# Performance work log

Measured on AMD Instinct MI355X. Metric: run time of the kernel, lower is better.

Reference implementation:

```python
import jax, jax.numpy as jnp
import numpy as np

B, T, C, H = 8, 2048, 1024, 128  # batch, seq (== block_size), embed_size, head_size


def setup_inputs() -> dict:
    key = jax.random.key(0)
    k1, k2, k3, k4 = jax.random.split(key, 4)
    x = jax.random.normal(k1, (B, T, C), dtype=jnp.float32)
    s = 1.0 / np.sqrt(C).astype(np.float32)
    Wq = jax.random.normal(k2, (C, H), dtype=jnp.float32) * s
    Wk = jax.random.normal(k3, (C, H), dtype=jnp.float32) * s
    Wv = jax.random.normal(k4, (C, H), dtype=jnp.float32) * s
    return {"x": x, "Wq": Wq, "Wk": Wk, "Wv": Wv}


def reference(x, Wq, Wk, Wv):
    # x: (B, T, C); projections are bias-free Linears -> x @ W
    Bs, Ts, Cs = x.shape
    q = x @ Wq  # (B, T, H)
    k = x @ Wk  # (B, T, H)
    v = x @ Wv  # (B, T, H)
    # NOTE: original scales by embed_size C ** -0.5, not head_size.
    sims = jnp.einsum('bth,bsh->bts', q, k) * (float(Cs) ** -0.5)  # (B, T, T)
    causal = jnp.tril(jnp.ones((Ts, Ts), dtype=bool))
    sims = jnp.where(causal[None, :, :], sims, -jnp.inf)
    attentions = jax.nn.softmax(sims, axis=-1)  # (B, T, T)
    return attentions @ v  # (B, T, H)
```

## Files before the change

kernel.cpp:

```cpp
#include <hip/hip_runtime.h>


#define B_ 8
#define T_ 2048
#define C_ 1024
#define H_ 128

typedef __attribute__((ext_vector_type(4))) float  f32x4;
typedef __attribute__((ext_vector_type(8))) __bf16 bf16x8;
typedef __attribute__((ext_vector_type(4))) __bf16 bf16x4;
typedef __attribute__((ext_vector_type(4))) short  short4v;

#define QSCALE (0.03125f * 1.44269504088896340736f)

static __device__ __forceinline__ short f2bf(float f) {
  union { __bf16 b; short s; } u;
  u.b = (__bf16)f;
  return u.s;
}

static __device__ __forceinline__ unsigned packbf2(float lo, float hi) {
  union { __bf16 b; unsigned short s; } a, c;
  a.b = (__bf16)lo; c.b = (__bf16)hi;
  return (unsigned)a.s | ((unsigned)c.s << 16);
}

static __device__ __forceinline__ size_t qk_idx(int t, int h, int nk) {
  return ((size_t)((t >> 4) * nk + (h >> 5)) << 9) + (((h >> 3) & 3) << 7)
       + ((t & 15) << 3) + (h & 7);
}
static __device__ __forceinline__ size_t v_idx(int h, int t) {
  return ((size_t)((t >> 4) * 8 + (h >> 4)) << 8) + ((h & 15) << 4) + (t & 15);
}

static __device__ __forceinline__ f32x4 mfma16(unsigned a0, unsigned a1,
                                               unsigned b0, unsigned b1, f32x4 c) {
#if __has_builtin(__builtin_amdgcn_mfma_f32_16x16x16_bf16)
  union { unsigned u[2]; bf16x4 v; } ua, ub;
  ua.u[0] = a0; ua.u[1] = a1; ub.u[0] = b0; ub.u[1] = b1;
  return __builtin_amdgcn_mfma_f32_16x16x16_bf16(ua.v, ub.v, c, 0, 0, 0);
#elif __has_builtin(__builtin_amdgcn_mfma_f32_16x16x16bf16_1k)
  union { unsigned u[2]; short4v v; } ua, ub;
  ua.u[0] = a0; ua.u[1] = a1; ub.u[0] = b0; ub.u[1] = b1;
  return __builtin_amdgcn_mfma_f32_16x16x16bf16_1k(ua.v, ub.v, c, 0, 0, 0);
#else
  union { unsigned u[2]; short4v v; } ua, ub;
  ua.u[0] = a0; ua.u[1] = a1; ub.u[0] = b0; ub.u[1] = b1;
  f32x4 d = c;
  asm volatile("v_mfma_f32_16x16x16_bf16 %0, %1, %2, %0"
               : "+v"(d) : "v"(ua.v), "v"(ub.v));
  return d;
#endif
}

__global__ void prep_wt(const float* __restrict__ Wq, const float* __restrict__ Wk,
                        const float* __restrict__ Wv, short* __restrict__ Wtf) {
  __shared__ float L[64 * 129];
  const int mtx = blockIdx.x >> 4, kc = blockIdx.x & 15;
  const int k0 = kc * 64;
  const float* W = (mtx == 0) ? Wq : (mtx == 1 ? Wk : Wv);
  const float s = (mtx == 0) ? QSCALE : 1.0f;
  for (int i = threadIdx.x; i < 64 * 128; i += 256) {
    int kk = i >> 7, c = i & 127;
    L[kk * 129 + c] = W[(size_t)(k0 + kk) * H_ + c] * s;
  }
  __syncthreads();
  for (int i = threadIdx.x; i < 128 * 64; i += 256) {
    int n = i >> 6, kk = i & 63;
    Wtf[qk_idx(mtx * 128 + n, k0 + kk, 32)] = f2bf(L[kk * 129 + n]);
  }
}

__global__ __launch_bounds__(256) void proj(const float* __restrict__ x,
                                            const short* __restrict__ Wtf,
                                            short* __restrict__ Qf,
                                            short* __restrict__ Kf,
                                            short* __restrict__ Vf) {
  __shared__ __align__(16) short At[2][64 * 256];
  const int tid = threadIdx.x, lane = tid & 63, wv = tid >> 6;
  const int cg = lane & 15, rg = lane >> 4;
  const int lane8 = lane << 3;
  const int g = (blockIdx.x & 7) * 64 + (blockIdx.x >> 3);
  const int mb = g >> 1, bn = g & 1;
  const int m0 = mb * 64;
  const int nfrag0 = bn * 12 + wv * 3;
  const float* xblk = x + (size_t)m0 * C_;

  f32x4 acc[4][3];
#pragma unroll
  for (int i = 0; i < 4; ++i)
#pragma unroll
    for (int j = 0; j < 3; ++j) {
      f32x4 z = {0.f, 0.f, 0.f, 0.f};
      acc[i][j] = z;
    }

  f32x4 ldr[8][2];

#define PLOAD(kt)                                                              \
  { _Pragma("unroll") for (int it = 0; it < 8; ++it) {                         \
      int ls = it * 256 + tid; int r = ls >> 5, sc = ls & 31;                  \
      const float* p = xblk + (size_t)r * C_ + (kt) * 256 + sc * 8;            \
      ldr[it][0] = *(const f32x4*)p; ldr[it][1] = *(const f32x4*)(p + 4);      \
  } }

#define PWRITE(bf)                                                             \
  { _Pragma("unroll") for (int it = 0; it < 8; ++it) {                         \
      int ls = it * 256 + tid; int r = ls >> 5, sc = ls & 31;                  \
      bf16x8 tv;                                                               \
      tv[0] = (__bf16)ldr[it][0][0]; tv[1] = (__bf16)ldr[it][0][1];            \
      tv[2] = (__bf16)ldr[it][0][2]; tv[3] = (__bf16)ldr[it][0][3];            \
      tv[4] = (__bf16)ldr[it][1][0]; tv[5] = (__bf16)ldr[it][1][1];            \
      tv[6] = (__bf16)ldr[it][1][2]; tv[7] = (__bf16)ldr[it][1][3];            \
      *(bf16x8*)&At[bf][r * 256 + ((sc ^ (r & 7)) << 3)] = tv;                 \
  } }

  PLOAD(0);
  PWRITE(0);
  __syncthreads();

  for (int kt = 0; kt < 4; ++kt) {
    const int cur = kt & 1;
    if (kt < 3) PLOAD(kt + 1);

#pragma unroll
    for (int ks = 0; ks < 8; ++ks) {
      bf16x8 af[4];
#pragma unroll
      for (int fm = 0; fm < 4; ++fm) {
        int r = fm * 16 + cg;
        int slot = (ks * 4 + rg) ^ (r & 7);
        af[fm] = *(const bf16x8*)&At[cur][r * 256 + (slot << 3)];
      }
#pragma unroll
      for (int nf = 0; nf < 3; ++nf) {
        bf16x8 bfr = *(const bf16x8*)&Wtf[((size_t)((nfrag0 + nf) * 32 + kt * 8 + ks) << 9) + lane8];
#pragma unroll
        for (int fm = 0; fm < 4; ++fm)
          acc[fm][nf] = __builtin_amdgcn_mfma_f32_16x16x32_bf16(af[fm], bfr, acc[fm][nf], 0, 0, 0);
      }
    }
    if (kt < 3) PWRITE(cur ^ 1);
    __syncthreads();
  }
#undef PLOAD
#undef PWRITE

#pragma unroll
  for (int fm = 0; fm < 4; ++fm) {
#pragma unroll
    for (int nf = 0; nf < 3; ++nf) {
      int n = (nfrag0 + nf) * 16 + cg;
      int rowm = m0 + fm * 16 + rg * 4;
      size_t boff = (size_t)(rowm >> 11) << 18;
      f32x4 v = acc[fm][nf];
      if (n < 128) {
#pragma unroll
        for (int r = 0; r < 4; ++r)
          Qf[boff + qk_idx((rowm + r) & 2047, n, 4)] = f2bf(v[r]);
      } else if (n < 256) {
#pragma unroll
        for (int r = 0; r < 4; ++r)
          Kf[boff + qk_idx((rowm + r) & 2047, n - 128, 4)] = f2bf(v[r]);
      } else {
#pragma unroll
        for (int r = 0; r < 4; ++r)
          Vf[boff + v_idx(n - 256, (rowm + r) & 2047)] = f2bf(v[r]);
      }
    }
  }
}

#define OCW 132
__global__ __launch_bounds__(512) void attn(const short* __restrict__ Qf,
                                            const short* __restrict__ Kf,
                                            const short* __restrict__ Vf,
                                            float* __restrict__ out) {
  __shared__ __align__(16) float OC[4][32 * OCW];
  __shared__ float Mml[8][32], Lml[8][32];
  const int tid = threadIdx.x, lane = tid & 63, wv = tid >> 6;
  const int cg = lane & 15, rg = lane >> 4;
  const int lane8 = lane << 3;
  const int bid = blockIdx.x;
  const int b = bid & 7;
  const int p = bid >> 3;
  const int grp = wv >> 2;
  const int wvl = wv & 3;
  const int qg = grp ? p : (63 - p);
  const int q0 = qg << 5;
  const int NT = (q0 + 95) >> 6;
  const int SPW = (NT + 3) >> 2;
  const int t0 = wvl * SPW;
  const int t1 = (t0 + SPW < NT) ? (t0 + SPW) : NT;

  const short* Qp = Qf + ((size_t)b << 18);
  const short* Kp = Kf + ((size_t)b << 18);
  const short* Vp = Vf + ((size_t)b << 18);
  const float NEG_INF = -__builtin_inff();

  bf16x8 qf[2][4];
#pragma unroll
  for (int qc = 0; qc < 2; ++qc)
#pragma unroll
    for (int ks = 0; ks < 4; ++ks)
      qf[qc][ks] = *(const bf16x8*)&Qp[((size_t)(((q0 >> 4) + qc) * 4 + ks) << 9) + lane8];

  f32x4 o[8][2];
#pragma unroll
  for (int f = 0; f < 8; ++f)
#pragma unroll
    for (int qc = 0; qc < 2; ++qc) { f32x4 z = {0.f, 0.f, 0.f, 0.f}; o[f][qc] = z; }
  float m[2] = {NEG_INF, NEG_INF}, lsum[2] = {0.0f, 0.0f};

  bf16x8 kf[4][4];
#define LOADK(t_)                                                              \
  { const short* ktp = Kp + (size_t)(t_) * 8192;                               \
    _Pragma("unroll") for (int nf_ = 0; nf_ < 4; ++nf_)                        \
    _Pragma("unroll") for (int ks_ = 0; ks_ < 4; ++ks_)                        \
      kf[nf_][ks_] = *(const bf16x8*)&ktp[((nf_ * 4 + ks_) << 9) + lane8]; }

  if (t0 < t1) LOADK(t0);

  for (int t = t0; t < t1; ++t) {
    const int kv0 = t * 64;
    const short* vtile = Vp + (size_t)t * 8192;

    f32x4 s[4][2];
#pragma unroll
    for (int nf = 0; nf < 4; ++nf)
#pragma unroll
      for (int qc = 0; qc < 2; ++qc) { f32x4 z = {0.f, 0.f, 0.f, 0.f}; s[nf][qc] = z; }

    __builtin_amdgcn_s_setprio(1);
#pragma unroll
    for (int nf = 0; nf < 4; ++nf)
#pragma unroll
      for (int ks = 0; ks < 4; ++ks) {
        s[nf][0] = __builtin_amdgcn_mfma_f32_16x16x32_bf16(kf[nf][ks], qf[0][ks], s[nf][0], 0, 0, 0);
        s[nf][1] = __builtin_amdgcn_mfma_f32_16x16x32_bf16(kf[nf][ks], qf[1][ks], s[nf][1], 0, 0, 0);
      }
    __builtin_amdgcn_s_setprio(0);

    if (t + 1 < t1) LOADK(t + 1);

    unsigned v0a[8], v0b[8];
#pragma unroll
    for (int hf = 0; hf < 8; ++hf) {
      const unsigned* vp = (const unsigned*)&vtile[(hf << 8) + (cg << 4) + (rg << 2)];
      v0a[hf] = vp[0]; v0b[hf] = vp[1];
    }

    if (t == NT - 1) {
#pragma unroll
      for (int nf = 0; nf < 4; ++nf)
#pragma unroll
        for (int qc = 0; qc < 2; ++qc)
#pragma unroll
          for (int r = 0; r < 4; ++r)
            if (kv0 + nf * 16 + rg * 4 + r > q0 + qc * 16 + cg) s[nf][qc][r] = NEG_INF;
    }

    unsigned pk[4][2][2];
#pragma unroll
    for (int qc = 0; qc < 2; ++qc) {
      float pm = s[0][qc][0];
#pragma unroll
      for (int nf = 0; nf < 4; ++nf)
#pragma unroll
        for (int r = 0; r < 4; ++r) pm = fmaxf(pm, s[nf][qc][r]);
      pm = fmaxf(pm, __shfl_xor(pm, 16));
      pm = fmaxf(pm, __shfl_xor(pm, 32));
      if (!__all(pm <= m[qc] + 8.0f)) {
        float mn = fmaxf(m[qc], pm);
        float sf = exp2f(m[qc] - mn);
        m[qc] = mn;
        lsum[qc] *= sf;
#pragma unroll
        for (int f = 0; f < 8; ++f)
#pragma unroll
          for (int r = 0; r < 4; ++r) o[f][qc][r] *= sf;
      }
      float mq = m[qc];
#pragma unroll
      for (int nf = 0; nf < 4; ++nf) {
        float p0 = exp2f(s[nf][qc][0] - mq), p1 = exp2f(s[nf][qc][1] - mq);
        float p2 = exp2f(s[nf][qc][2] - mq), p3 = exp2f(s[nf][qc][3] - mq);
        lsum[qc] += (p0 + p1) + (p2 + p3);
        pk[nf][qc][0] = packbf2(p0, p1);
        pk[nf][qc][1] = packbf2(p2, p3);
      }
    }

    __builtin_amdgcn_s_setprio(1);
#pragma unroll
    for (int hf = 0; hf < 8; ++hf) {
      o[hf][0] = mfma16(v0a[hf], v0b[hf], pk[0][0][0], pk[0][0][1], o[hf][0]);
      o[hf][1] = mfma16(v0a[hf], v0b[hf], pk[0][1][0], pk[0][1][1], o[hf][1]);
    }
#pragma unroll
    for (int nf = 1; nf < 4; ++nf) {
      const unsigned b00 = pk[nf][0][0], b01 = pk[nf][0][1];
      const unsigned b10 = pk[nf][1][0], b11 = pk[nf][1][1];
#pragma unroll
      for (int hf = 0; hf < 8; ++hf) {
        const unsigned* vp = (const unsigned*)&vtile[((nf * 8 + hf) << 8) + (cg << 4) + (rg << 2)];
        unsigned v0 = vp[0], v1 = vp[1];
        o[hf][0] = mfma16(v0, v1, b00, b01, o[hf][0]);
        o[hf][1] = mfma16(v0, v1, b10, b11, o[hf][1]);
      }
    }
    __builtin_amdgcn_s_setprio(0);
  }
#undef LOADK

#pragma unroll
  for (int qc = 0; qc < 2; ++qc) {
    lsum[qc] += __shfl_xor(lsum[qc], 16);
    lsum[qc] += __shfl_xor(lsum[qc], 32);
  }
  if (lane < 16) {
#pragma unroll
    for (int qc = 0; qc < 2; ++qc) {
      Mml[wv][qc * 16 + lane] = m[qc];
      Lml[wv][qc * 16 + lane] = lsum[qc];
    }
  }
  if (grp == 0) {
#pragma unroll
    for (int hf = 0; hf < 8; ++hf)
#pragma unroll
      for (int qc = 0; qc < 2; ++qc)
        *(f32x4*)&OC[wv][(qc * 16 + cg) * OCW + hf * 16 + rg * 4] = o[hf][qc];
  }
  __syncthreads();
  {
    const int qb = (63 - p) << 5;
    for (int i = tid; i < 32 * 128; i += 512) {
      int row = i >> 7, col = i & 127;
      float ms = fmaxf(fmaxf(Mml[0][row], Mml[1][row]), fmaxf(Mml[2][row], Mml[3][row]));
      float accv = 0.f, lacc = 0.f;
#pragma unroll
      for (int w = 0; w < 4; ++w) {
        float sc = exp2f(Mml[w][row] - ms);
        lacc += sc * Lml[w][row];
        accv += sc * OC[w][row * OCW + col];
      }
      out[(size_t)(b * T_ + qb + row) * H_ + col] = accv / lacc;
    }
  }
  __syncthreads();
  if (grp == 1) {
#pragma unroll
    for (int hf = 0; hf < 8; ++hf)
#pragma unroll
      for (int qc = 0; qc < 2; ++qc)
        *(f32x4*)&OC[wvl][(qc * 16 + cg) * OCW + hf * 16 + rg * 4] = o[hf][qc];
  }
  __syncthreads();
  {
    const int qb = p << 5;
    for (int i = tid; i < 32 * 128; i += 512) {
      int row = i >> 7, col = i & 127;
      float ms = fmaxf(fmaxf(Mml[4][row], Mml[5][row]), fmaxf(Mml[6][row], Mml[7][row]));
      float accv = 0.f, lacc = 0.f;
#pragma unroll
      for (int w = 0; w < 4; ++w) {
        float sc = exp2f(Mml[4 + w][row] - ms);
        lacc += sc * Lml[4 + w][row];
        accv += sc * OC[w][row * OCW + col];
      }
      out[(size_t)(b * T_ + qb + row) * H_ + col] = accv / lacc;
    }
  }
}

extern "C" void kernel_launch(void* const* d_in, const int* in_sizes, int n_in,
                              void* d_out, int out_size, void* d_ws, size_t ws_size,
                              hipStream_t stream) {
  const float* x  = (const float*)d_in[0];
  const float* Wq = (const float*)d_in[1];
  const float* Wk = (const float*)d_in[2];
  const float* Wv = (const float*)d_in[3];
  float* out = (float*)d_out;
  char* ws = (char*)d_ws;

  short* Wtf = (short*)(ws);
  short* Qf  = (short*)(ws + ((size_t)1 << 20));
  short* Kf  = (short*)(ws + ((size_t)5 << 20));
  short* Vf  = (short*)(ws + ((size_t)9 << 20));

  prep_wt<<<dim3(48), dim3(256), 0, stream>>>(Wq, Wk, Wv, Wtf);
  proj<<<dim3(512), dim3(256), 0, stream>>>(x, Wtf, Qf, Kf, Vf);
  attn<<<dim3(256), dim3(512), 0, stream>>>(Qf, Kf, Vf, out);
}
```

Before: 79.83 us.

## Pre-convert x to bf16 fragment layout in separate kernel, stream MFMA operands from global

Adds an xconv kernel that converts x to bf16 once and stores it in MFMA-fragment order in the workspace. The projection kernel then drops its LDS staging and barriers and loads A/B fragments directly from global memory, double-buffered in registers, with s_setprio around the MFMA blocks. Launch bounds now request two blocks per SM. The intent is to remove LDS traffic and synchronisation from the projection and to stop each column-half block converting the same x tile. The cost is an extra kernel launch plus a 32 MB bf16 write and read-back of x.

```diff
diff --git a/kernel.cpp b/kernel.cpp
--- a/kernel.cpp
+++ b/kernel.cpp
@@ -71,12 +71,32 @@
   }
 }
 
-__global__ __launch_bounds__(256) void proj(const float* __restrict__ x,
-                                            const short* __restrict__ Wtf,
-                                            short* __restrict__ Qf,
-                                            short* __restrict__ Kf,
-                                            short* __restrict__ Vf) {
-  __shared__ __align__(16) short At[2][64 * 256];
+__global__ __launch_bounds__(256) void xconv(const float* __restrict__ x,
+                                             short* __restrict__ Xf) {
+  const int lane = threadIdx.x & 63;
+  const int cg = lane & 15, rg = lane >> 4;
+  const int w = (blockIdx.x << 2) + (threadIdx.x >> 6);
+#pragma unroll
+  for (int i = 0; i < 8; ++i) {
+    int f = (w << 3) + i;
+    int t16 = f >> 5, ks = f & 31;
+    const float* p = x + ((size_t)(t16 * 16 + cg)) * C_ + ks * 32 + rg * 8;
+    f32x4 v0 = *(const f32x4*)p;
+    f32x4 v1 = *(const f32x4*)(p + 4);
+    bf16x8 t;
+    t[0] = (__bf16)v0[0]; t[1] = (__bf16)v0[1];
+    t[2] = (__bf16)v0[2]; t[3] = (__bf16)v0[3];
+    t[4] = (__bf16)v1[0]; t[5] = (__bf16)v1[1];
+    t[6] = (__bf16)v1[2]; t[7] = (__bf16)v1[3];
+    *(bf16x8*)&Xf[((size_t)f << 9) + (lane << 3)] = t;
+  }
+}
+
+__global__ __launch_bounds__(256, 2) void proj(const short* __restrict__ Xf,
+                                               const short* __restrict__ Wtf,
+                                               short* __restrict__ Qf,
+                                               short* __restrict__ Kf,
+                                               short* __restrict__ Vf) {
   const int tid = threadIdx.x, lane = tid & 63, wv = tid >> 6;
   const int cg = lane & 15, rg = lane >> 4;
   const int lane8 = lane << 3;
@@ -84,7 +104,6 @@
   const int mb = g >> 1, bn = g & 1;
   const int m0 = mb * 64;
   const int nfrag0 = bn * 12 + wv * 3;
-  const float* xblk = x + (size_t)m0 * C_;
 
   f32x4 acc[4][3];
 #pragma unroll
@@ -95,56 +114,35 @@
       acc[i][j] = z;
     }
 
-  f32x4 ldr[8][2];
-
-#define PLOAD(kt)                                                              \
-  { _Pragma("unroll") for (int it = 0; it < 8; ++it) {                         \
-      int ls = it * 256 + tid; int r = ls >> 5, sc = ls & 31;                  \
-      const float* p = xblk + (size_t)r * C_ + (kt) * 256 + sc * 8;            \
-      ldr[it][0] = *(const f32x4*)p; ldr[it][1] = *(const f32x4*)(p + 4);      \
-  } }
-
-#define PWRITE(bf)                                                             \
-  { _Pragma("unroll") for (int it = 0; it < 8; ++it) {                         \
-      int ls = it * 256 + tid; int r = ls >> 5, sc = ls & 31;                  \
-      bf16x8 tv;                                                               \
-      tv[0] = (__bf16)ldr[it][0][0]; tv[1] = (__bf16)ldr[it][0][1];            \
-      tv[2] = (__bf16)ldr[it][0][2]; tv[3] = (__bf16)ldr[it][0][3];            \
-      tv[4] = (__bf16)ldr[it][1][0]; tv[5] = (__bf16)ldr[it][1][1];            \
-      tv[6] = (__bf16)ldr[it][1][2]; tv[7] = (__bf16)ldr[it][1][3];            \
-      *(bf16x8*)&At[bf][r * 256 + ((sc ^ (r & 7)) << 3)] = tv;                 \
-  } }
-
-  PLOAD(0);
-  PWRITE(0);
-  __syncthreads();
-
-  for (int kt = 0; kt < 4; ++kt) {
-    const int cur = kt & 1;
-    if (kt < 3) PLOAD(kt + 1);
-
-#pragma unroll
-    for (int ks = 0; ks < 8; ++ks) {
-      bf16x8 af[4];
-#pragma unroll
-      for (int fm = 0; fm < 4; ++fm) {
-        int r = fm * 16 + cg;
-        int slot = (ks * 4 + rg) ^ (r & 7);
-        af[fm] = *(const bf16x8*)&At[cur][r * 256 + (slot << 3)];
-      }
-#pragma unroll
-      for (int nf = 0; nf < 3; ++nf) {
-        bf16x8 bfr = *(const bf16x8*)&Wtf[((size_t)((nfrag0 + nf) * 32 + kt * 8 + ks) << 9) + lane8];
-#pragma unroll
-        for (int fm = 0; fm < 4; ++fm)
-          acc[fm][nf] = __builtin_amdgcn_mfma_f32_16x16x32_bf16(af[fm], bfr, acc[fm][nf], 0, 0, 0);
-      }
-    }
-    if (kt < 3) PWRITE(cur ^ 1);
-    __syncthreads();
-  }
-#undef PLOAD
-#undef PWRITE
+  bf16x8 A0[4], B0[3], A1[4], B1[3];
+
+#define LDA(dst, ks)                                                           \
+  { _Pragma("unroll") for (int fm = 0; fm < 4; ++fm)                           \
+      dst[fm] = *(const bf16x8*)&Xf[(((size_t)(mb * 4 + fm) * 32 + (ks)) << 9) + lane8]; }
+#define LDB(dst, ks)                                                           \
+  { _Pragma("unroll") for (int nf = 0; nf < 3; ++nf)                           \
+      dst[nf] = *(const bf16x8*)&Wtf[(((size_t)(nfrag0 + nf) * 32 + (ks)) << 9) + lane8]; }
+#define MM(Aa, Bb)                                                             \
+  { _Pragma("unroll") for (int nf = 0; nf < 3; ++nf)                           \
+    _Pragma("unroll") for (int fm = 0; fm < 4; ++fm)                           \
+      acc[fm][nf] = __builtin_amdgcn_mfma_f32_16x16x32_bf16(Aa[fm], Bb[nf], acc[fm][nf], 0, 0, 0); }
+
+  LDA(A0, 0); LDB(B0, 0);
+  LDA(A1, 1); LDB(B1, 1);
+#pragma unroll
+  for (int ks = 0; ks < 32; ks += 2) {
+    __builtin_amdgcn_s_setprio(1);
+    MM(A0, B0);
+    __builtin_amdgcn_s_setprio(0);
+    if (ks + 2 < 32) { LDA(A0, ks + 2); LDB(B0, ks + 2); }
+    __builtin_amdgcn_s_setprio(1);
+    MM(A1, B1);
+    __builtin_amdgcn_s_setprio(0);
+    if (ks + 3 < 32) { LDA(A1, ks + 3); LDB(B1, ks + 3); }
+  }
+#undef LDA
+#undef LDB
+#undef MM
 
 #pragma unroll
   for (int fm = 0; fm < 4; ++fm) {
@@ -388,8 +386,10 @@
   short* Qf  = (short*)(ws + ((size_t)1 << 20));
   short* Kf  = (short*)(ws + ((size_t)5 << 20));
   short* Vf  = (short*)(ws + ((size_t)9 << 20));
+  short* Xf  = (short*)(ws + ((size_t)13 << 20));
 
   prep_wt<<<dim3(48), dim3(256), 0, stream>>>(Wq, Wk, Wv, Wtf);
-  proj<<<dim3(512), dim3(256), 0, stream>>>(x, Wtf, Qf, Kf, Vf);
+  xconv<<<dim3(1024), dim3(256), 0, stream>>>(x, Xf);
+  proj<<<dim3(512), dim3(256), 0, stream>>>(Xf, Wtf, Qf, Kf, Vf);
   attn<<<dim3(256), dim3(512), 0, stream>>>(Qf, Kf, Vf, out);
 }
```

New measurement: 80.48 us. No clear change (+0.8%).
